# Optimization experiments

Measured on AMD Instinct MI355X. Metric: run time of the kernel, lower is better.

The kernel has to match this reference:

```python
import jax, jax.numpy as jnp
import numpy as np

B, M, R = 2, 2048, 256
H, DH = 16, 64
ROPE_THETA = 10000.0


def setup_inputs() -> dict:
    key = jax.random.key(0)
    ks = jax.random.split(key, 9)
    d = H * DH
    inp = {
        "Pq": jax.random.normal(ks[0], (B, M, R), jnp.float32),
        "Pk": jax.random.normal(ks[1], (B, M, R), jnp.float32),
        "Pv": jax.random.normal(ks[2], (B, M, R), jnp.float32),
        "Vq": jax.random.normal(ks[3], (R, d), jnp.float32) / np.sqrt(R),
        "Vk": jax.random.normal(ks[4], (R, d), jnp.float32) / np.sqrt(R),
        "Vv": jax.random.normal(ks[5], (R, d), jnp.float32) / np.sqrt(R),
        "bq": jax.random.normal(ks[6], (d,), jnp.float32),
        "bk": jax.random.normal(ks[7], (d,), jnp.float32),
        "bv": jax.random.normal(ks[8], (d,), jnp.float32),
        "attention_mask": jnp.ones((B, M), jnp.int32),
        "position_ids": jnp.tile(jnp.arange(M, dtype=jnp.int32), (B, 1)),
    }
    return inp


def _rope_cos_sin(position_ids):
    # half-half RoPE tables; kernel only reads the first half of cos/sin
    inv_freq = 1.0 / (ROPE_THETA ** (jnp.arange(0, DH, 2, dtype=jnp.float32) / DH))
    freqs = position_ids.astype(jnp.float32)[:, :, None] * inv_freq[None, None, :]  # [B,M,DH/2]
    return jnp.cos(freqs)[:, None], jnp.sin(freqs)[:, None]  # [B,1,M,DH/2]


def _heads(P, V, b):
    # low-rank reconstruction: [B,M,R] @ [R,H*DH] + [H*DH] -> [B,H,M,DH]
    x = jnp.einsum('bmr,rd->bmd', P, V) + b
    return x.reshape(x.shape[0], x.shape[1], H, DH).transpose(0, 2, 1, 3)


def _rotate(x, cos, sin):
    x0, x1 = x[..., :DH // 2], x[..., DH // 2:]
    return jnp.concatenate([x0 * cos - x1 * sin, x0 * sin + x1 * cos], axis=-1)


def reference(Pq, Pk, Pv, Vq, Vk, Vv, bq, bk, bv, attention_mask, position_ids):
    cos, sin = _rope_cos_sin(position_ids)
    q = _rotate(_heads(Pq, Vq, bq), cos, sin)  # [B,H,M,DH]
    k = _rotate(_heads(Pk, Vk, bk), cos, sin)
    v = _heads(Pv, Vv, bv)
    scale = 1.0 / jnp.sqrt(jnp.float32(DH))
    scores = jnp.einsum('bhmd,bhnd->bhmn', q, k) * scale
    keep = attention_mask.astype(bool)[:, None, None, :]
    scores = jnp.where(keep, scores, -jnp.inf)
    # online-softmax equivalent with all-masked-row zeroing (matches kernel)
    mx = jnp.max(scores, axis=-1, keepdims=True)
    safe_mx = jnp.where(jnp.isfinite(mx), mx, 0.0)
    p = jnp.exp(scores - safe_mx)
    l = jnp.sum(p, axis=-1, keepdims=True)
    out = jnp.einsum('bhmn,bhnd->bhmd', p, v) / jnp.where(l > 0, l, 1.0)
    out = jnp.where(l > 0, out, 0.0)
    return out  # [B,H,M,DH]
```

## Files before the change

### kernel.cpp

```cpp
#include <hip/hip_runtime.h>
#include <cstdint>
#include <cstddef>

#define Bc 2
#define Mc 2048
#define Rc 256
#define Hc 16
#define DHc 64
#define Dc (Hc * DHc)
#define NKT (Mc / 64)

typedef __attribute__((ext_vector_type(8))) short short8;
typedef __attribute__((ext_vector_type(4))) float float4v;
typedef __attribute__((ext_vector_type(4))) unsigned short ushort4v;
typedef __attribute__((ext_vector_type(4))) unsigned int uint4v;

__device__ inline unsigned short f2bf(float f) {
    union { float f; uint32_t u; } v;
    v.f = f;
    uint32_t r = v.u + 0x7fffu + ((v.u >> 16) & 1u);
    return (unsigned short)(r >> 16);
}

__global__ __launch_bounds__(256)
void transpose_v(const float* __restrict__ V0, const float* __restrict__ V1,
                 const float* __restrict__ V2, unsigned short* __restrict__ Vt)
{
    const int mat = blockIdx.z;
    const float* src = mat == 0 ? V0 : (mat == 1 ? V1 : V2);
    const int d  = blockIdx.x * 256 + threadIdx.x;
    const int kg = blockIdx.y;
    short8 v;
    #pragma unroll
    for (int j = 0; j < 8; ++j)
        v[j] = (short)f2bf(src[(size_t)(kg * 8 + j) * Dc + d]);
    *(short8*)&Vt[((size_t)mat * Dc + d) * Rc + kg * 8] = v;
}

__global__ __launch_bounds__(256)
void proj_kernel(const float* __restrict__ P,
                 const unsigned short* __restrict__ Vt,
                 const float* __restrict__ bias,
                 const int* __restrict__ pos_ids,
                 unsigned short* __restrict__ out,
                 int do_rope)
{
    __shared__ __align__(16) unsigned short As[64][136];
    __shared__ __align__(16) unsigned short Bs[64][136];

    const int tid = threadIdx.x;
    const int m0  = blockIdx.x * 64;
    const int h   = blockIdx.y;
    const int b   = blockIdx.z;

    const int w    = tid >> 6;
    const int lane = tid & 63;
    const int col  = lane & 15;
    const int quad = lane >> 4;

    const float* Pblk = P + ((size_t)b * Mc + m0) * Rc;

    float4v acc[4] = {};

    for (int ko = 0; ko < Rc; ko += 128) {
        __syncthreads();
        #pragma unroll
        for (int i = 0; i < 8; ++i) {
            int idx = tid + i * 256;
            int row = idx >> 5;
            int c4  = idx & 31;
            float4 f = *((const float4*)(Pblk + (size_t)row * Rc + ko) + c4);
            ushort4v u = { f2bf(f.x), f2bf(f.y), f2bf(f.z), f2bf(f.w) };
            *(ushort4v*)&As[row][c4 * 4] = u;
        }
        const unsigned short* Vh = Vt + (size_t)h * DHc * Rc + ko;
        #pragma unroll
        for (int i = 0; i < 4; ++i) {
            int idx = tid + i * 256;
            int row = idx >> 4, c8 = idx & 15;
            *(short8*)&Bs[row][c8 * 8] = *(const short8*)&Vh[(size_t)row * Rc + c8 * 8];
        }
        __syncthreads();

        #pragma unroll
        for (int kk = 0; kk < 4; ++kk) {
            short8 a = *(const short8*)&As[w * 16 + col][kk * 32 + quad * 8];
            #pragma unroll
            for (int c = 0; c < 4; ++c) {
                short8 bf = *(const short8*)&Bs[c * 16 + col][kk * 32 + quad * 8];
                acc[c] = __builtin_amdgcn_mfma_f32_16x16x32_bf16(a, bf, acc[c], 0, 0, 0);
            }
        }
    }

    const int mrow0 = m0 + w * 16 + quad * 4;

    if (do_rope) {
        #pragma unroll
        for (int c = 0; c < 2; ++c) {
            int j = c * 16 + col;
            float b0 = bias[h * DHc + j];
            float b1 = bias[h * DHc + j + 32];
            float inv_freq = __expf(-0.28782314f * (float)j);
            #pragma unroll
            for (int r = 0; r < 4; ++r) {
                int m = mrow0 + r;
                float pos = (float)pos_ids[b * Mc + m];
                float ang = pos * inv_freq;
                float cs = __cosf(ang), sn = __sinf(ang);
                float x0 = acc[c][r] + b0;
                float x1 = acc[c + 2][r] + b1;
                size_t base = ((size_t)(b * Hc + h) * Mc + m) * DHc;
                out[base + j]      = f2bf(x0 * cs - x1 * sn);
                out[base + j + 32] = f2bf(x0 * sn + x1 * cs);
            }
        }
    } else {
        #pragma unroll
        for (int c = 0; c < 4; ++c) {
            int dh = c * 16 + col;
            float bb = bias[h * DHc + dh];
            ushort4v v;
            #pragma unroll
            for (int r = 0; r < 4; ++r) v[r] = f2bf(acc[c][r] + bb);
            size_t base = ((size_t)(b * Hc + h) * DHc + dh) * Mc + mrow0;
            *(ushort4v*)&out[base] = v;
        }
    }
}

__global__ __launch_bounds__(256)
void attn_kernel(const unsigned short* __restrict__ Qb,
                 const unsigned short* __restrict__ Kb,
                 const unsigned short* __restrict__ Vt,
                 const int* __restrict__ mask,
                 float* __restrict__ out)
{
    __shared__ __align__(16) unsigned short Ks[64][72];
    __shared__ __align__(16) unsigned short Vs[64][72];
    __shared__ __align__(16) unsigned short Ps[4][16][72];

    const int tid = threadIdx.x;
    const int q0  = blockIdx.x * 64;
    const int bh  = blockIdx.y;
    const int b   = bh >> 4;

    const int w    = tid >> 6;
    const int lane = tid & 63;
    const int col  = lane & 15;
    const int quad = lane >> 4;

    const unsigned short* Qg = Qb + ((size_t)bh * Mc + q0 + w * 16 + col) * DHc;
    const short8 qf0 = *(const short8*)&Qg[quad * 8];
    const short8 qf1 = *(const short8*)&Qg[32 + quad * 8];

    const int srow = tid >> 3, sc8 = tid & 7;
    const unsigned short* Kg = Kb + (size_t)bh * Mc * DHc;
    const unsigned short* Vg = Vt + (size_t)bh * DHc * Mc;
    const int4* mp = (const int4*)(mask + b * Mc);

    uint4v kreg0 = *(const uint4v*)&Kg[(size_t)srow * DHc + sc8 * 8];
    uint4v kreg1 = *(const uint4v*)&Kg[(size_t)(srow + 32) * DHc + sc8 * 8];
    uint4v vreg0 = *(const uint4v*)&Vg[(size_t)srow * Mc + sc8 * 8];
    uint4v vreg1 = *(const uint4v*)&Vg[(size_t)(srow + 32) * Mc + sc8 * 8];

    float lsum = 0.0f;
    float4v acc_o[4] = {};

    for (int kb = 0; kb < NKT; ++kb) {
        __syncthreads();
        *(uint4v*)&Ks[srow][sc8 * 8]      = kreg0;
        *(uint4v*)&Ks[srow + 32][sc8 * 8] = kreg1;
        *(uint4v*)&Vs[srow][sc8 * 8]      = vreg0;
        *(uint4v*)&Vs[srow + 32][sc8 * 8] = vreg1;
        __syncthreads();

        if (kb + 1 < NKT) {
            const unsigned short* Kn = Kg + (size_t)(kb + 1) * 64 * DHc;
            kreg0 = *(const uint4v*)&Kn[(size_t)srow * DHc + sc8 * 8];
            kreg1 = *(const uint4v*)&Kn[(size_t)(srow + 32) * DHc + sc8 * 8];
            vreg0 = *(const uint4v*)&Vg[(size_t)srow * Mc + (kb + 1) * 64 + sc8 * 8];
            vreg1 = *(const uint4v*)&Vg[(size_t)(srow + 32) * Mc + (kb + 1) * 64 + sc8 * 8];
        }

        int4 mv[4];
        #pragma unroll
        for (int c = 0; c < 4; ++c) mv[c] = mp[kb * 16 + c * 4 + quad];

        #pragma unroll
        for (int c = 0; c < 4; ++c) {
            float4v sacc = {};
            short8 a0 = *(const short8*)&Ks[c * 16 + col][quad * 8];
            short8 a1 = *(const short8*)&Ks[c * 16 + col][32 + quad * 8];
            sacc = __builtin_amdgcn_mfma_f32_16x16x32_bf16(a0, qf0, sacc, 0, 0, 0);
            sacc = __builtin_amdgcn_mfma_f32_16x16x32_bf16(a1, qf1, sacc, 0, 0, 0);

            const int* mi = (const int*)&mv[c];
            ushort4v pw;
            #pragma unroll
            for (int r = 0; r < 4; ++r) {
                float madd = mi[r] ? -20.0f : -1e30f;
                float p = __expf(fmaf(sacc[r], 0.125f, madd));
                lsum += p;
                pw[r] = f2bf(p);
            }
            *(ushort4v*)&Ps[w][col][c * 16 + quad * 4] = pw;
        }

        #pragma unroll
        for (int kk = 0; kk < 2; ++kk) {
            short8 a = *(const short8*)&Ps[w][col][kk * 32 + quad * 8];
            #pragma unroll
            for (int c = 0; c < 4; ++c) {
                short8 bf = *(const short8*)&Vs[c * 16 + col][kk * 32 + quad * 8];
                acc_o[c] = __builtin_amdgcn_mfma_f32_16x16x32_bf16(a, bf, acc_o[c], 0, 0, 0);
            }
        }
    }

    lsum += __shfl_xor(lsum, 16);
    lsum += __shfl_xor(lsum, 32);

    #pragma unroll
    for (int r = 0; r < 4; ++r) {
        float lr  = __shfl(lsum, quad * 4 + r);
        float inv = (lr > 0.0f) ? 1.0f / lr : 0.0f;
        int m = q0 + w * 16 + quad * 4 + r;
        float* og = out + ((size_t)bh * Mc + m) * DHc;
        #pragma unroll
        for (int c = 0; c < 4; ++c) og[c * 16 + col] = acc_o[c][r] * inv;
    }
}

extern "C" void kernel_launch(void* const* d_in, const int* in_sizes, int n_in,
                              void* d_out, int out_size, void* d_ws, size_t ws_size,
                              hipStream_t stream) {
    const float* Pq = (const float*)d_in[0];
    const float* Pk = (const float*)d_in[1];
    const float* Pv = (const float*)d_in[2];
    const float* Vq = (const float*)d_in[3];
    const float* Vk = (const float*)d_in[4];
    const float* Vv = (const float*)d_in[5];
    const float* bq = (const float*)d_in[6];
    const float* bk = (const float*)d_in[7];
    const float* bv = (const float*)d_in[8];
    const int*   am = (const int*)d_in[9];
    const int*   pid = (const int*)d_in[10];
    float* out = (float*)d_out;

    const size_t n_el = (size_t)Bc * Hc * Mc * DHc;
    unsigned short* Qb = (unsigned short*)d_ws;
    unsigned short* Kb = Qb + n_el;
    unsigned short* Vta = Kb + n_el;
    unsigned short* Vtp = Vta + n_el;

    dim3 blk(256);
    transpose_v<<<dim3(Dc / 256, Rc / 8, 3), blk, 0, stream>>>(Vq, Vk, Vv, Vtp);

    dim3 gA(Mc / 64, Hc, Bc);
    proj_kernel<<<gA, blk, 0, stream>>>(Pq, Vtp,                 bq, pid, Qb, 1);
    proj_kernel<<<gA, blk, 0, stream>>>(Pk, Vtp + (size_t)Dc * Rc, bk, pid, Kb, 1);
    proj_kernel<<<gA, blk, 0, stream>>>(Pv, Vtp + 2 * (size_t)Dc * Rc, bv, pid, Vta, 0);

    dim3 gB(Mc / 64, Bc * Hc);
    attn_kernel<<<gB, blk, 0, stream>>>(Qb, Kb, Vta, am, out);
}
```

Measured before the change: 180.6 us.

## Restructure projection and attention with larger tiles, swizzled LDS, and precomputed tables

New measurement: 167.4 us. 1.08x faster.

```diff
diff --git a/kernel.cpp b/kernel.cpp
--- a/kernel.cpp
+++ b/kernel.cpp
@@ -15,11 +15,41 @@
 typedef __attribute__((ext_vector_type(4))) unsigned short ushort4v;
 typedef __attribute__((ext_vector_type(4))) unsigned int uint4v;
 
+#if __has_builtin(__builtin_amdgcn_exp2f)
+#define EXPFN(x) __builtin_amdgcn_exp2f(x)
+#define QSCALE 0.18033688f
+#define MADD_KEEP (-28.8539008f)
+#else
+#define EXPFN(x) __expf(x)
+#define QSCALE 0.125f
+#define MADD_KEEP (-20.0f)
+#endif
+
 __device__ inline unsigned short f2bf(float f) {
     union { float f; uint32_t u; } v;
     v.f = f;
     uint32_t r = v.u + 0x7fffu + ((v.u >> 16) & 1u);
     return (unsigned short)(r >> 16);
+}
+
+__device__ inline int swz(int row, int chunk) {
+    return row * 128 + ((chunk ^ (row & 7)) << 4);
+}
+
+__global__ __launch_bounds__(256)
+void convP(const float* __restrict__ P0, const float* __restrict__ P1,
+           const float* __restrict__ P2, unsigned short* __restrict__ Pb)
+{
+    const int mat = blockIdx.y;
+    const float* src = mat == 0 ? P0 : (mat == 1 ? P1 : P2);
+    size_t idx = ((size_t)blockIdx.x * 256 + threadIdx.x) * 8;
+    float4 f0 = *(const float4*)&src[idx];
+    float4 f1 = *(const float4*)&src[idx + 4];
+    ushort4v a = { f2bf(f0.x), f2bf(f0.y), f2bf(f0.z), f2bf(f0.w) };
+    ushort4v c = { f2bf(f1.x), f2bf(f1.y), f2bf(f1.z), f2bf(f1.w) };
+    unsigned short* dst = Pb + (size_t)mat * Bc * Mc * Rc + idx;
+    *(ushort4v*)dst = a;
+    *(ushort4v*)(dst + 4) = c;
 }
 
 __global__ __launch_bounds__(256)
@@ -38,198 +68,240 @@
 }
 
 __global__ __launch_bounds__(256)
-void proj_kernel(const float* __restrict__ P,
-                 const unsigned short* __restrict__ Vt,
-                 const float* __restrict__ bias,
-                 const int* __restrict__ pos_ids,
-                 unsigned short* __restrict__ out,
-                 int do_rope)
-{
-    __shared__ __align__(16) unsigned short As[64][136];
-    __shared__ __align__(16) unsigned short Bs[64][136];
+void rope_madd(const int* __restrict__ pos_ids, const int* __restrict__ mask,
+               float2* __restrict__ ropetab, float* __restrict__ maddf)
+{
+    int row = blockIdx.x * 8 + (threadIdx.x >> 5);
+    int j = threadIdx.x & 31;
+    float inv = __expf(-0.28782314f * (float)j);
+    float ang = (float)pos_ids[row] * inv;
+    ropetab[(size_t)row * 32 + j] = make_float2(__cosf(ang), __sinf(ang));
+    if (j == 0) maddf[row] = mask[row] ? MADD_KEEP : -1e30f;
+}
+
+__global__ __launch_bounds__(256, 2)
+void proj_kernel(const unsigned short* __restrict__ Pb,
+                 const unsigned short* __restrict__ Vtp,
+                 const float* __restrict__ bq, const float* __restrict__ bk,
+                 const float* __restrict__ bv,
+                 const float2* __restrict__ ropetab,
+                 unsigned short* __restrict__ Qb, unsigned short* __restrict__ Kb,
+                 unsigned short* __restrict__ Vta)
+{
+    __shared__ __align__(16) unsigned char AtB[128 * 128];
+    __shared__ __align__(16) unsigned char BtB[128 * 128];
 
     const int tid = threadIdx.x;
-    const int m0  = blockIdx.x * 64;
-    const int h   = blockIdx.y;
-    const int b   = blockIdx.z;
-
-    const int w    = tid >> 6;
-    const int lane = tid & 63;
-    const int col  = lane & 15;
-    const int quad = lane >> 4;
-
-    const float* Pblk = P + ((size_t)b * Mc + m0) * Rc;
-
-    float4v acc[4] = {};
-
-    for (int ko = 0; ko < Rc; ko += 128) {
+    const int z = blockIdx.z, mat = z >> 1, b = z & 1;
+    const int m0 = blockIdx.x * 128, d0 = blockIdx.y * 128;
+    const int w = tid >> 6, lane = tid & 63, col = lane & 15, quad = lane >> 4;
+    const int mh = w & 1, dh2 = w >> 1;
+
+    const unsigned short* Pg = Pb + ((size_t)mat * Bc + b) * Mc * Rc + (size_t)m0 * Rc;
+    const unsigned short* Vg = Vtp + (size_t)mat * Dc * Rc + (size_t)d0 * Rc;
+
+    const int srow = tid >> 1, sc0 = (tid & 1) * 4;
+
+    float4v acc[4][4] = {};
+
+    for (int kc = 0; kc < 4; ++kc) {
+        uint4v ar[4], br[4];
+        #pragma unroll
+        for (int i = 0; i < 4; ++i) {
+            ar[i] = *(const uint4v*)&Pg[(size_t)srow * Rc + kc * 64 + (sc0 + i) * 8];
+            br[i] = *(const uint4v*)&Vg[(size_t)srow * Rc + kc * 64 + (sc0 + i) * 8];
+        }
         __syncthreads();
         #pragma unroll
-        for (int i = 0; i < 8; ++i) {
-            int idx = tid + i * 256;
-            int row = idx >> 5;
-            int c4  = idx & 31;
-            float4 f = *((const float4*)(Pblk + (size_t)row * Rc + ko) + c4);
-            ushort4v u = { f2bf(f.x), f2bf(f.y), f2bf(f.z), f2bf(f.w) };
-            *(ushort4v*)&As[row][c4 * 4] = u;
-        }
-        const unsigned short* Vh = Vt + (size_t)h * DHc * Rc + ko;
-        #pragma unroll
         for (int i = 0; i < 4; ++i) {
-            int idx = tid + i * 256;
-            int row = idx >> 4, c8 = idx & 15;
-            *(short8*)&Bs[row][c8 * 8] = *(const short8*)&Vh[(size_t)row * Rc + c8 * 8];
+            *(uint4v*)(AtB + swz(srow, sc0 + i)) = ar[i];
+            *(uint4v*)(BtB + swz(srow, sc0 + i)) = br[i];
         }
         __syncthreads();
 
         #pragma unroll
-        for (int kk = 0; kk < 4; ++kk) {
-            short8 a = *(const short8*)&As[w * 16 + col][kk * 32 + quad * 8];
-            #pragma unroll
-            for (int c = 0; c < 4; ++c) {
-                short8 bf = *(const short8*)&Bs[c * 16 + col][kk * 32 + quad * 8];
-                acc[c] = __builtin_amdgcn_mfma_f32_16x16x32_bf16(a, bf, acc[c], 0, 0, 0);
-            }
-        }
-    }
-
-    const int mrow0 = m0 + w * 16 + quad * 4;
-
-    if (do_rope) {
-        #pragma unroll
-        for (int c = 0; c < 2; ++c) {
-            int j = c * 16 + col;
-            float b0 = bias[h * DHc + j];
-            float b1 = bias[h * DHc + j + 32];
-            float inv_freq = __expf(-0.28782314f * (float)j);
+        for (int kk = 0; kk < 2; ++kk) {
+            short8 af[4], bf[4];
+            #pragma unroll
+            for (int mt = 0; mt < 4; ++mt)
+                af[mt] = *(const short8*)(AtB + swz(mh * 64 + mt * 16 + col, kk * 4 + quad));
+            #pragma unroll
+            for (int dt = 0; dt < 4; ++dt)
+                bf[dt] = *(const short8*)(BtB + swz(dh2 * 64 + dt * 16 + col, kk * 4 + quad));
+            #pragma unroll
+            for (int mt = 0; mt < 4; ++mt)
+                #pragma unroll
+                for (int dt = 0; dt < 4; ++dt)
+                    acc[mt][dt] = __builtin_amdgcn_mfma_f32_16x16x32_bf16(
+                        af[mt], bf[dt], acc[mt][dt], 0, 0, 0);
+        }
+    }
+
+    const int head = (d0 + dh2 * 64) >> 6;
+    const int bh = b * Hc + head;
+
+    if (mat < 2) {
+        const float* bias = mat == 0 ? bq : bk;
+        unsigned short* outp = mat == 0 ? Qb : Kb;
+        const float oscale = mat == 0 ? QSCALE : 1.0f;
+        float b00 = bias[head * 64 + col],      b01 = bias[head * 64 + 16 + col];
+        float b10 = bias[head * 64 + 32 + col], b11 = bias[head * 64 + 48 + col];
+        #pragma unroll
+        for (int mt = 0; mt < 4; ++mt)
             #pragma unroll
             for (int r = 0; r < 4; ++r) {
-                int m = mrow0 + r;
-                float pos = (float)pos_ids[b * Mc + m];
-                float ang = pos * inv_freq;
-                float cs = __cosf(ang), sn = __sinf(ang);
-                float x0 = acc[c][r] + b0;
-                float x1 = acc[c + 2][r] + b1;
-                size_t base = ((size_t)(b * Hc + h) * Mc + m) * DHc;
-                out[base + j]      = f2bf(x0 * cs - x1 * sn);
-                out[base + j + 32] = f2bf(x0 * sn + x1 * cs);
-            }
-        }
+                int m = m0 + mh * 64 + mt * 16 + quad * 4 + r;
+                float2 cs0 = ropetab[((size_t)b * Mc + m) * 32 + col];
+                float2 cs1 = ropetab[((size_t)b * Mc + m) * 32 + 16 + col];
+                float x00 = acc[mt][0][r] + b00, x10 = acc[mt][2][r] + b10;
+                float x01 = acc[mt][1][r] + b01, x11 = acc[mt][3][r] + b11;
+                unsigned short* og = outp + ((size_t)bh * Mc + m) * DHc;
+                og[col]      = f2bf((x00 * cs0.x - x10 * cs0.y) * oscale);
+                og[32 + col] = f2bf((x00 * cs0.y + x10 * cs0.x) * oscale);
+                og[16 + col] = f2bf((x01 * cs1.x - x11 * cs1.y) * oscale);
+                og[48 + col] = f2bf((x01 * cs1.y + x11 * cs1.x) * oscale);
+            }
     } else {
         #pragma unroll
-        for (int c = 0; c < 4; ++c) {
-            int dh = c * 16 + col;
-            float bb = bias[h * DHc + dh];
-            ushort4v v;
-            #pragma unroll
-            for (int r = 0; r < 4; ++r) v[r] = f2bf(acc[c][r] + bb);
-            size_t base = ((size_t)(b * Hc + h) * DHc + dh) * Mc + mrow0;
-            *(ushort4v*)&out[base] = v;
-        }
-    }
-}
-
-__global__ __launch_bounds__(256)
+        for (int dt = 0; dt < 4; ++dt) {
+            int d = d0 + dh2 * 64 + dt * 16 + col;
+            float bb = bv[d];
+            int dh = d & 63;
+            #pragma unroll
+            for (int mt = 0; mt < 4; ++mt) {
+                ushort4v pv;
+                #pragma unroll
+                for (int r = 0; r < 4; ++r) pv[r] = f2bf(acc[mt][dt][r] + bb);
+                size_t base = ((size_t)bh * DHc + dh) * Mc + m0 + mh * 64 + mt * 16 + quad * 4;
+                *(ushort4v*)&Vta[base] = pv;
+            }
+        }
+    }
+}
+
+__global__ __launch_bounds__(256, 2)
 void attn_kernel(const unsigned short* __restrict__ Qb,
                  const unsigned short* __restrict__ Kb,
                  const unsigned short* __restrict__ Vt,
-                 const int* __restrict__ mask,
+                 const float* __restrict__ maddf,
                  float* __restrict__ out)
 {
-    __shared__ __align__(16) unsigned short Ks[64][72];
-    __shared__ __align__(16) unsigned short Vs[64][72];
-    __shared__ __align__(16) unsigned short Ps[4][16][72];
+    __shared__ __align__(16) unsigned char KsB[64 * 128];
+    __shared__ __align__(16) unsigned char VsB[64 * 128];
+    __shared__ __align__(16) unsigned short Ps[4][32][72];
 
     const int tid = threadIdx.x;
-    const int q0  = blockIdx.x * 64;
-    const int bh  = blockIdx.y;
-    const int b   = bh >> 4;
-
-    const int w    = tid >> 6;
-    const int lane = tid & 63;
-    const int col  = lane & 15;
-    const int quad = lane >> 4;
-
-    const unsigned short* Qg = Qb + ((size_t)bh * Mc + q0 + w * 16 + col) * DHc;
-    const short8 qf0 = *(const short8*)&Qg[quad * 8];
-    const short8 qf1 = *(const short8*)&Qg[32 + quad * 8];
-
-    const int srow = tid >> 3, sc8 = tid & 7;
+    const int q0 = blockIdx.x * 128;
+    const int bh = blockIdx.y;
+    const int b  = bh >> 4;
+    const int w = tid >> 6, lane = tid & 63, col = lane & 15, quad = lane >> 4;
+
+    short8 qf[2][2];
+    #pragma unroll
+    for (int qs = 0; qs < 2; ++qs) {
+        const unsigned short* Qg =
+            Qb + ((size_t)bh * Mc + q0 + w * 32 + qs * 16 + col) * DHc + quad * 8;
+        qf[qs][0] = *(const short8*)Qg;
+        qf[qs][1] = *(const short8*)(Qg + 32);
+    }
+
+    const int srow = tid >> 3, sc = tid & 7;
+    const int dst0 = swz(srow, sc), dst1 = swz(srow + 32, sc);
     const unsigned short* Kg = Kb + (size_t)bh * Mc * DHc;
     const unsigned short* Vg = Vt + (size_t)bh * DHc * Mc;
-    const int4* mp = (const int4*)(mask + b * Mc);
-
-    uint4v kreg0 = *(const uint4v*)&Kg[(size_t)srow * DHc + sc8 * 8];
-    uint4v kreg1 = *(const uint4v*)&Kg[(size_t)(srow + 32) * DHc + sc8 * 8];
-    uint4v vreg0 = *(const uint4v*)&Vg[(size_t)srow * Mc + sc8 * 8];
-    uint4v vreg1 = *(const uint4v*)&Vg[(size_t)(srow + 32) * Mc + sc8 * 8];
-
-    float lsum = 0.0f;
-    float4v acc_o[4] = {};
-
-    for (int kb = 0; kb < NKT; ++kb) {
+    const float* mdp = maddf + b * Mc;
+
+    uint4v kr0 = *(const uint4v*)&Kg[(size_t)srow * DHc + sc * 8];
+    uint4v kr1 = *(const uint4v*)&Kg[(size_t)(srow + 32) * DHc + sc * 8];
+    uint4v vr0 = *(const uint4v*)&Vg[(size_t)srow * Mc + sc * 8];
+    uint4v vr1 = *(const uint4v*)&Vg[(size_t)(srow + 32) * Mc + sc * 8];
+
+    float lsum[2] = {0.0f, 0.0f};
+    float4v acc_o[2][4] = {};
+
+    for (int kt = 0; kt < NKT; ++kt) {
         __syncthreads();
-        *(uint4v*)&Ks[srow][sc8 * 8]      = kreg0;
-        *(uint4v*)&Ks[srow + 32][sc8 * 8] = kreg1;
-        *(uint4v*)&Vs[srow][sc8 * 8]      = vreg0;
-        *(uint4v*)&Vs[srow + 32][sc8 * 8] = vreg1;
+        *(uint4v*)(KsB + dst0) = kr0; *(uint4v*)(KsB + dst1) = kr1;
+        *(uint4v*)(VsB + dst0) = vr0; *(uint4v*)(VsB + dst1) = vr1;
         __syncthreads();
 
-        if (kb + 1 < NKT) {
-            const unsigned short* Kn = Kg + (size_t)(kb + 1) * 64 * DHc;
-            kreg0 = *(const uint4v*)&Kn[(size_t)srow * DHc + sc8 * 8];
-            kreg1 = *(const uint4v*)&Kn[(size_t)(srow + 32) * DHc + sc8 * 8];
-            vreg0 = *(const uint4v*)&Vg[(size_t)srow * Mc + (kb + 1) * 64 + sc8 * 8];
-            vreg1 = *(const uint4v*)&Vg[(size_t)(srow + 32) * Mc + (kb + 1) * 64 + sc8 * 8];
-        }
-
-        int4 mv[4];
-        #pragma unroll
-        for (int c = 0; c < 4; ++c) mv[c] = mp[kb * 16 + c * 4 + quad];
-
-        #pragma unroll
-        for (int c = 0; c < 4; ++c) {
-            float4v sacc = {};
-            short8 a0 = *(const short8*)&Ks[c * 16 + col][quad * 8];
-            short8 a1 = *(const short8*)&Ks[c * 16 + col][32 + quad * 8];
-            sacc = __builtin_amdgcn_mfma_f32_16x16x32_bf16(a0, qf0, sacc, 0, 0, 0);
-            sacc = __builtin_amdgcn_mfma_f32_16x16x32_bf16(a1, qf1, sacc, 0, 0, 0);
-
-            const int* mi = (const int*)&mv[c];
-            ushort4v pw;
-            #pragma unroll
-            for (int r = 0; r < 4; ++r) {
-                float madd = mi[r] ? -20.0f : -1e30f;
-                float p = __expf(fmaf(sacc[r], 0.125f, madd));
-                lsum += p;
-                pw[r] = f2bf(p);
-            }
-            *(ushort4v*)&Ps[w][col][c * 16 + quad * 4] = pw;
+        if (kt + 1 < NKT) {
+            const unsigned short* Kn = Kg + (size_t)(kt + 1) * 64 * DHc;
+            kr0 = *(const uint4v*)&Kn[(size_t)srow * DHc + sc * 8];
+            kr1 = *(const uint4v*)&Kn[(size_t)(srow + 32) * DHc + sc * 8];
+            vr0 = *(const uint4v*)&Vg[(size_t)srow * Mc + (kt + 1) * 64 + sc * 8];
+            vr1 = *(const uint4v*)&Vg[(size_t)(srow + 32) * Mc + (kt + 1) * 64 + sc * 8];
+        }
+
+        float4 md[4];
+        #pragma unroll
+        for (int ks = 0; ks < 4; ++ks)
+            md[ks] = *(const float4*)&mdp[kt * 64 + ks * 16 + quad * 4];
+
+        float4v sacc[4][2] = {};
+        #pragma unroll
+        for (int ks = 0; ks < 4; ++ks) {
+            short8 a0 = *(const short8*)(KsB + swz(ks * 16 + col, quad));
+            short8 a1 = *(const short8*)(KsB + swz(ks * 16 + col, 4 + quad));
+            #pragma unroll
+            for (int qs = 0; qs < 2; ++qs) {
+                sacc[ks][qs] = __builtin_amdgcn_mfma_f32_16x16x32_bf16(
+                    a0, qf[qs][0], sacc[ks][qs], 0, 0, 0);
+                sacc[ks][qs] = __builtin_amdgcn_mfma_f32_16x16x32_bf16(
+                    a1, qf[qs][1], sacc[ks][qs], 0, 0, 0);
+            }
+        }
+
+        #pragma unroll
+        for (int ks = 0; ks < 4; ++ks) {
+            const float* mdk = (const float*)&md[ks];
+            #pragma unroll
+            for (int qs = 0; qs < 2; ++qs) {
+                ushort4v pw;
+                #pragma unroll
+                for (int r = 0; r < 4; ++r) {
+                    float p = EXPFN(sacc[ks][qs][r] + mdk[r]);
+                    lsum[qs] += p;
+                    union { float f; uint32_t u; } cv; cv.f = p;
+                    pw[r] = (unsigned short)((cv.u + 0x8000u) >> 16);
+                }
+                *(ushort4v*)&Ps[w][qs * 16 + col][ks * 16 + quad * 4] = pw;
+            }
         }
 
         #pragma unroll
         for (int kk = 0; kk < 2; ++kk) {
-            short8 a = *(const short8*)&Ps[w][col][kk * 32 + quad * 8];
-            #pragma unroll
-            for (int c = 0; c < 4; ++c) {
-                short8 bf = *(const short8*)&Vs[c * 16 + col][kk * 32 + quad * 8];
-                acc_o[c] = __builtin_amdgcn_mfma_f32_16x16x32_bf16(a, bf, acc_o[c], 0, 0, 0);
-            }
-        }
-    }
-
-    lsum += __shfl_xor(lsum, 16);
-    lsum += __shfl_xor(lsum, 32);
+            short8 pa0 = *(const short8*)&Ps[w][col][kk * 32 + quad * 8];
+            short8 pa1 = *(const short8*)&Ps[w][16 + col][kk * 32 + quad * 8];
+            #pragma unroll
+            for (int ds = 0; ds < 4; ++ds) {
+                short8 vb = *(const short8*)(VsB + swz(ds * 16 + col, kk * 4 + quad));
+                acc_o[0][ds] = __builtin_amdgcn_mfma_f32_16x16x32_bf16(
+                    pa0, vb, acc_o[0][ds], 0, 0, 0);
+                acc_o[1][ds] = __builtin_amdgcn_mfma_f32_16x16x32_bf16(
+                    pa1, vb, acc_o[1][ds], 0, 0, 0);
+            }
+        }
+    }
 
     #pragma unroll
-    for (int r = 0; r < 4; ++r) {
-        float lr  = __shfl(lsum, quad * 4 + r);
-        float inv = (lr > 0.0f) ? 1.0f / lr : 0.0f;
-        int m = q0 + w * 16 + quad * 4 + r;
-        float* og = out + ((size_t)bh * Mc + m) * DHc;
-        #pragma unroll
-        for (int c = 0; c < 4; ++c) og[c * 16 + col] = acc_o[c][r] * inv;
-    }
+    for (int qs = 0; qs < 2; ++qs) {
+        lsum[qs] += __shfl_xor(lsum[qs], 16);
+        lsum[qs] += __shfl_xor(lsum[qs], 32);
+    }
+
+    #pragma unroll
+    for (int qs = 0; qs < 2; ++qs)
+        #pragma unroll
+        for (int r = 0; r < 4; ++r) {
+            float lr = __shfl(lsum[qs], quad * 4 + r);
+            float inv = (lr > 0.0f) ? 1.0f / lr : 0.0f;
+            int m = q0 + w * 32 + qs * 16 + quad * 4 + r;
+            float* og = out + ((size_t)bh * Mc + m) * DHc;
+            #pragma unroll
+            for (int ds = 0; ds < 4; ++ds)
+                og[ds * 16 + col] = acc_o[qs][ds][r] * inv;
+        }
 }
 
 extern "C" void kernel_launch(void* const* d_in, const int* in_sizes, int n_in,
@@ -249,19 +321,21 @@
     float* out = (float*)d_out;
 
     const size_t n_el = (size_t)Bc * Hc * Mc * DHc;
-    unsigned short* Qb = (unsigned short*)d_ws;
-    unsigned short* Kb = Qb + n_el;
+    unsigned short* Qb  = (unsigned short*)d_ws;
+    unsigned short* Kb  = Qb + n_el;
     unsigned short* Vta = Kb + n_el;
-    unsigned short* Vtp = Vta + n_el;
+    unsigned short* Pb  = Vta + n_el;
+    unsigned short* Vtp = Pb + (size_t)3 * Bc * Mc * Rc;
+    float2* ropetab = (float2*)(Vtp + (size_t)3 * Dc * Rc);
+    float*  maddf   = (float*)(ropetab + (size_t)Bc * Mc * 32);
 
     dim3 blk(256);
+    convP<<<dim3((Bc * Mc * Rc) / 8 / 256, 3), blk, 0, stream>>>(Pq, Pk, Pv, Pb);
     transpose_v<<<dim3(Dc / 256, Rc / 8, 3), blk, 0, stream>>>(Vq, Vk, Vv, Vtp);
-
-    dim3 gA(Mc / 64, Hc, Bc);
-    proj_kernel<<<gA, blk, 0, stream>>>(Pq, Vtp,                 bq, pid, Qb, 1);
-    proj_kernel<<<gA, blk, 0, stream>>>(Pk, Vtp + (size_t)Dc * Rc, bk, pid, Kb, 1);
-    proj_kernel<<<gA, blk, 0, stream>>>(Pv, Vtp + 2 * (size_t)Dc * Rc, bv, pid, Vta, 0);
-
-    dim3 gB(Mc / 64, Bc * Hc);
-    attn_kernel<<<gB, blk, 0, stream>>>(Qb, Kb, Vta, am, out);
-}
+    rope_madd<<<dim3(Bc * Mc / 8), blk, 0, stream>>>(pid, am, ropetab, maddf);
+
+    proj_kernel<<<dim3(Mc / 128, Dc / 128, 6), blk, 0, stream>>>(
+        Pb, Vtp, bq, bk, bv, ropetab, Qb, Kb, Vta);
+
+    attn_kernel<<<dim3(Mc / 128, Bc * Hc), blk, 0, stream>>>(Qb, Kb, Vta, maddf, out);
+}
```
